# Kernel tuning notes

Hardware: AMD Instinct MI355X
Metric: run time of the kernel (lower is better)

## Reference

```python
import jax, jax.numpy as jnp
import numpy as np

BITS = 4
N_PACK = 32 // BITS  # int32 compression
GROUPSIZE = 128
MASK = (1 << BITS) - 1


def _unpack_int32(q, axis):
    """Unpack int32 tensor into N_PACK low-bit values along `axis`.
    Element j*N_PACK+e comes from bits [BITS*e, BITS*(e+1)) of packed word j."""
    parts = [ (q >> (BITS * e)) & MASK for e in range(N_PACK) ]
    u = jnp.stack(parts, axis=axis + 1)  # (..., P, N_PACK, ...)
    shape = list(q.shape)
    shape[axis] = shape[axis] * N_PACK
    return u.reshape(shape)


def setup_inputs() -> dict:
    key = jax.random.key(0)
    k1, k2, k3, k4, k5 = jax.random.split(key, 5)
    in_f, out_f = 4096, 12288
    tokens = 8192
    n_groups = in_f // GROUPSIZE  # 32
    x = jax.random.normal(k1, (tokens, in_f), dtype=jnp.float32)
    scales = jax.random.uniform(k2, (n_groups, out_f), dtype=jnp.float32) * 0.01 + 1e-3
    bias = jax.random.normal(k3, (out_f,), dtype=jnp.float32)
    qweight = jax.random.randint(k4, (in_f // N_PACK, out_f), jnp.iinfo(jnp.int32).min, jnp.iinfo(jnp.int32).max, dtype=jnp.int32)
    qzeros = jax.random.randint(k5, (n_groups, out_f // N_PACK), jnp.iinfo(jnp.int32).min, jnp.iinfo(jnp.int32).max, dtype=jnp.int32)
    return {"x": x, "scales": scales, "bias": bias, "qweight": qweight, "qzeros": qzeros}


def reference(x, scales, bias, qweight, qzeros):
    in_f = qweight.shape[0] * N_PACK
    out_f = qweight.shape[1]
    n_groups = scales.shape[0]
    # Unpack 4-bit weights along input-channel axis: (in_f, out_f), values 0..15
    w_int = _unpack_int32(qweight, axis=0).astype(scales.dtype)
    # Unpack zero points along output-channel axis; optimum format stores zp-1
    zp = (_unpack_int32(qzeros, axis=1) + 1).astype(scales.dtype)  # (n_groups, out_f)
    # Per-group dequant: group g covers input channels [g*GROUPSIZE, (g+1)*GROUPSIZE)
    w = (w_int.reshape(n_groups, GROUPSIZE, out_f) - zp[:, None, :]) * scales[:, None, :]
    w = w.reshape(in_f, out_f)
    # Linear: y = x @ W^T with W = w.T, i.e. x @ w
    return x @ w + bias
```

## Files before the change

kernel.cpp:

```cpp
#include <hip/hip_runtime.h>
#include <hip/hip_bf16.h>


typedef __attribute__((ext_vector_type(8))) short short8;
typedef __attribute__((ext_vector_type(4))) float f32x4;

__device__ __forceinline__ short f2bf(float f) {
  unsigned u = __float_as_uint(f);
  u += 0x7fffu + ((u >> 16) & 1u);
  return (short)(u >> 16);
}

__device__ __forceinline__ void gload_lds16(const void* g, void* l) {
  __builtin_amdgcn_global_load_lds(
      (const __attribute__((address_space(1))) void*)g,
      (__attribute__((address_space(3))) void*)l,
      16, 0, 0);
}

__device__ __forceinline__ void bar() {
  asm volatile("" ::: "memory");
  __builtin_amdgcn_s_barrier();
  asm volatile("" ::: "memory");
}

__global__ __launch_bounds__(256) void dequant_tile_kernel(
    const int* __restrict__ qweight, const int* __restrict__ qzeros,
    const float* __restrict__ scales, short* __restrict__ Bt,
    int N, int K) {
  const int ktn = K >> 5;
  const int bx = blockIdx.x;
  const int nb = bx / ktn, kt = bx - nb * ktn;
  const int t = threadIdx.x;
  const int g = kt >> 2;
  char* dst = (char*)Bt + (size_t)bx * 8192;
#pragma unroll
  for (int p = 0; p < 2; ++p) {
    const int c = p * 256 + t;
    const int l = c & 63;
    const int n = nb * 128 + (c >> 6) * 16 + (l & 15);
    const int kw = kt * 4 + (l >> 4);
    const float sc = scales[(size_t)g * N + n];
    const int zw = qzeros[(size_t)g * (N >> 3) + (n >> 3)];
    const float zs = -(float)(((zw >> ((n & 7) * 4)) & 15) + 1) * sc;
    const int w = qweight[(size_t)kw * N + n];
    short8 v;
#pragma unroll
    for (int e = 0; e < 8; ++e)
      v[e] = f2bf(fmaf((float)((w >> (4 * e)) & 15), sc, zs));
    *(short8*)(dst + c * 16) = v;
  }
}

__global__ __launch_bounds__(256) void cvt_tile_kernel(
    const float* __restrict__ x, short* __restrict__ xb, int K) {
  const int ktn = K >> 5;
  const int bx = blockIdx.x;
  const int mb = bx / ktn, kt = bx - mb * ktn;
  char* dst = (char*)xb + (size_t)bx * 16384;
#pragma unroll
  for (int p = 0; p < 4; ++p) {
    const int c = p * 256 + threadIdx.x;
    const int l = c & 63;
    const int row = mb * 256 + (c >> 6) * 16 + (l & 15);
    const int k = kt * 32 + (l >> 4) * 8;
    const float* s = x + (size_t)row * K + k;
    float4 f0 = *(const float4*)s;
    float4 f1 = *(const float4*)(s + 4);
    short8 v;
    v[0] = f2bf(f0.x); v[1] = f2bf(f0.y); v[2] = f2bf(f0.z); v[3] = f2bf(f0.w);
    v[4] = f2bf(f1.x); v[5] = f2bf(f1.y); v[6] = f2bf(f1.z); v[7] = f2bf(f1.w);
    *(short8*)(dst + c * 16) = v;
  }
}

#define GBM 256
#define GBN 128

__global__ __launch_bounds__(512, 4) void gemm256_kernel(
    const short* __restrict__ At, const short* __restrict__ Bt,
    const float* __restrict__ bias, float* __restrict__ C,
    int M, int N, int K) {
  __shared__ __align__(16) char lds[3 * 16384];
  const int tid = threadIdx.x;
  const int nbx = N / GBN;
  const int nwg = gridDim.x;
  int bid = blockIdx.x;
  if ((nwg & 7) == 0) bid = (bid & 7) * (nwg >> 3) + (bid >> 3);
  const int mb = bid / nbx;
  const int nb = bid % nbx;
  const int bm = mb * GBM, bn = nb * GBN;

  const int wid = tid >> 6, lane = tid & 63;
  const int wr = wid >> 1, wc = wid & 1;

  const int P = K >> 5;

  char* lb = &lds[0];

  const char* aBase = lb + wr * 4096 + lane * 16;

  const char* pA = (const char*)At + (size_t)mb * P * 16384 + (size_t)tid * 16;
  char* dA = lb + tid * 16;

  const char* pB = (const char*)Bt + (size_t)nb * P * 8192 + wc * 4096 +
                   (size_t)lane * 16;

  short8 bs[2][4];

#define STAGE(TSL, AOFF)                                 \
  do {                                                   \
    gload_lds16(pA + (AOFF), dA + (TSL)*16384);          \
    gload_lds16(pA + (AOFF) + 8192, dA + (TSL)*16384 + 8192); \
  } while (0)

#define LOADB(SET, BOFF)                                             \
  do {                                                               \
    asm volatile("global_load_dwordx4 %0, %1, off"                   \
                 : "=v"(bs[SET][0]) : "v"(pB + (BOFF)));             \
    asm volatile("global_load_dwordx4 %0, %1, off"                   \
                 : "=v"(bs[SET][1]) : "v"(pB + (BOFF) + 1024));      \
    asm volatile("global_load_dwordx4 %0, %1, off"                   \
                 : "=v"(bs[SET][2]) : "v"(pB + (BOFF) + 2048));      \
    asm volatile("global_load_dwordx4 %0, %1, off"                   \
                 : "=v"(bs[SET][3]) : "v"(pB + (BOFF) + 3072));      \
  } while (0)

#define WAITB(NSTR, SET)                                                   \
  asm volatile("s_waitcnt vmcnt(" NSTR ")"                                 \
               : "+v"(bs[SET][0]), "+v"(bs[SET][1]), "+v"(bs[SET][2]),     \
                 "+v"(bs[SET][3])::"memory")

  short8 aR[4];

#define RDA(SL)                                                   \
  do {                                                            \
    _Pragma("unroll") for (int i = 0; i < 4; ++i) aR[i] =         \
        *(const short8*)(aBase + (SL)*16384 + i * 1024);          \
  } while (0)

  f32x4 acc[4][4] = {};

#define MFMA16(SET)                                                      \
  do {                                                                   \
    __builtin_amdgcn_s_setprio(1);                                       \
    _Pragma("unroll") for (int i = 0; i < 4; ++i)                        \
        _Pragma("unroll") for (int j = 0; j < 4; ++j) acc[i][j] =        \
            __builtin_amdgcn_mfma_f32_16x16x32_bf16(aR[i], bs[SET][j],   \
                                                    acc[i][j], 0, 0, 0); \
    __builtin_amdgcn_s_setprio(0);                                       \
  } while (0)

#define PHASE(SL, SET, R)                                  \
  do {                                                     \
    WAITB("2", SET);                                       \
    bar();                                                 \
    RDA(SL);                                               \
    LOADB((SET) ^ 1, ((R) + 1) * 8192);                    \
    STAGE(((SL) + 2) % 3, ((R) + 2) * 16384);              \
    MFMA16(SET);                                           \
  } while (0)

  STAGE(0, 0);
  LOADB(0, 0);
  STAGE(1, 16384);

  const int nIt = (P - 2) / 6;
  for (int it = 0; it < nIt; ++it) {
    PHASE(0, 0, 0);
    PHASE(1, 1, 1);
    PHASE(2, 0, 2);
    PHASE(0, 1, 3);
    PHASE(1, 0, 4);
    PHASE(2, 1, 5);
    pA += 6 * 16384;
    pB += 6 * 8192;
  }
  WAITB("2", 0);
  bar();
  RDA(0);
  LOADB(1, 1 * 8192);
  MFMA16(0);
  WAITB("0", 1);
  bar();
  RDA(1);
  MFMA16(1);

#undef PHASE
#undef MFMA16
#undef RDA
#undef WAITB
#undef LOADB
#undef STAGE

  const int crow0 = bm + wr * 64 + (lane >> 4) * 4;
  const int ccol0 = bn + wc * 64 + (lane & 15);
#pragma unroll
  for (int fj = 0; fj < 4; ++fj) {
    const float bv = bias[ccol0 + fj * 16];
#pragma unroll
    for (int fi = 0; fi < 4; ++fi) {
#pragma unroll
      for (int r = 0; r < 4; ++r) {
        C[(size_t)(crow0 + fi * 16 + r) * N + ccol0 + fj * 16] =
            acc[fi][fj][r] + bv;
      }
    }
  }
}

__global__ __launch_bounds__(256) void dequant_kernel(
    const int* __restrict__ qweight, const int* __restrict__ qzeros,
    const float* __restrict__ scales, short* __restrict__ Wt,
    int in_f, int out_f) {
  __shared__ __align__(16) short T[64][72];
  const int n0 = blockIdx.x * 64;
  const int k0 = blockIdx.y * 64;
  const int t = threadIdx.x;
  const int nl = t & 63;
  const int kw = t >> 6;
  const int n = n0 + nl;
  const int g = k0 >> 7;
  const float sc = scales[(size_t)g * out_f + n];
  const int zpw = qzeros[(size_t)g * (out_f >> 3) + (n >> 3)];
  const float zp = (float)(((zpw >> ((n & 7) * 4)) & 15) + 1);
  const float zs = zp * sc;
#pragma unroll
  for (int rr = 0; rr < 2; ++rr) {
    const int kwi = kw + rr * 4;
    const int w = qweight[(size_t)((k0 >> 3) + kwi) * out_f + n];
    short8 v;
#pragma unroll
    for (int e = 0; e < 8; ++e) {
      float f = (float)((w >> (4 * e)) & 15) * sc - zs;
      v[e] = f2bf(f);
    }
    *(short8*)&T[nl][kwi * 8] = v;
  }
  __syncthreads();
#pragma unroll
  for (int rr = 0; rr < 2; ++rr) {
    const int c = rr * 256 + t;
    const int row = c >> 3, ch = c & 7;
    *(short8*)&Wt[(size_t)(n0 + row) * in_f + k0 + ch * 8] =
        *(const short8*)&T[row][ch * 8];
  }
}

__global__ __launch_bounds__(256) void cvt_kernel(
    const float* __restrict__ x, short* __restrict__ xb, long n8) {
  long i = (long)blockIdx.x * blockDim.x + threadIdx.x;
  if (i >= n8) return;
  const float* src = x + i * 8;
  float4 a = *(const float4*)src;
  float4 b = *(const float4*)(src + 4);
  short8 v;
  v[0] = f2bf(a.x); v[1] = f2bf(a.y); v[2] = f2bf(a.z); v[3] = f2bf(a.w);
  v[4] = f2bf(b.x); v[5] = f2bf(b.y); v[6] = f2bf(b.z); v[7] = f2bf(b.w);
  *(short8*)(xb + i * 8) = v;
}

#define BM 128
#define BN 128
#define BK 64

template <bool A_BF16>
__global__ __launch_bounds__(256) void gemm_bias_kernel(
    const void* __restrict__ Av, const short* __restrict__ Bt,
    const float* __restrict__ bias, float* __restrict__ C,
    int M, int N, int K) {
  __shared__ __align__(16) short As[BM * BK];
  __shared__ __align__(16) short Bs[BN * BK];
  const int tid = threadIdx.x;
  const int bm = blockIdx.y * BM;
  const int bn = blockIdx.x * BN;
  const int wid = tid >> 6, lane = tid & 63;
  const int wr = wid >> 1, wc = wid & 1;
  const int lrow = lane & 15;
  const int lk = (lane >> 4) * 8;

  f32x4 acc[4][4] = {};

  for (int kt = 0; kt < K; kt += BK) {
    if constexpr (A_BF16) {
      const short* A = (const short*)Av;
#pragma unroll
      for (int r = 0; r < 4; ++r) {
        const int c = r * 256 + tid;
        const int row = c >> 3, ch = c & 7;
        gload_lds16(A + (size_t)(bm + row) * K + kt + ch * 8,
                    (char*)As + c * 16);
      }
    } else {
      const float* A = (const float*)Av;
#pragma unroll
      for (int r = 0; r < 4; ++r) {
        const int c = r * 256 + tid;
        const int row = c >> 3, ch = c & 7;
        const float* src = A + (size_t)(bm + row) * K + kt + ch * 8;
        float4 f0 = *(const float4*)src;
        float4 f1 = *(const float4*)(src + 4);
        short8 v;
        v[0] = f2bf(f0.x); v[1] = f2bf(f0.y); v[2] = f2bf(f0.z); v[3] = f2bf(f0.w);
        v[4] = f2bf(f1.x); v[5] = f2bf(f1.y); v[6] = f2bf(f1.z); v[7] = f2bf(f1.w);
        *(short8*)((char*)As + c * 16) = v;
      }
    }
#pragma unroll
    for (int r = 0; r < 4; ++r) {
      const int c = r * 256 + tid;
      const int row = c >> 3, ch = c & 7;
      gload_lds16(Bt + (size_t)(bn + row) * K + kt + ch * 8,
                  (char*)Bs + c * 16);
    }
    __syncthreads();
#pragma unroll
    for (int kk = 0; kk < 2; ++kk) {
      short8 af[4], bf[4];
#pragma unroll
      for (int i = 0; i < 4; ++i)
        af[i] = *(const short8*)&As[(wr * 64 + i * 16 + lrow) * BK + kk * 32 + lk];
#pragma unroll
      for (int j = 0; j < 4; ++j)
        bf[j] = *(const short8*)&Bs[(wc * 64 + j * 16 + lrow) * BK + kk * 32 + lk];
#pragma unroll
      for (int i = 0; i < 4; ++i)
#pragma unroll
        for (int j = 0; j < 4; ++j)
          acc[i][j] = __builtin_amdgcn_mfma_f32_16x16x32_bf16(
              af[i], bf[j], acc[i][j], 0, 0, 0);
    }
    __syncthreads();
  }

  const int crow0 = bm + wr * 64 + (lane >> 4) * 4;
  const int ccol0 = bn + wc * 64 + (lane & 15);
#pragma unroll
  for (int j = 0; j < 4; ++j) {
    const float bv = bias[ccol0 + j * 16];
#pragma unroll
    for (int i = 0; i < 4; ++i) {
#pragma unroll
      for (int r = 0; r < 4; ++r) {
        C[(size_t)(crow0 + i * 16 + r) * N + ccol0 + j * 16] = acc[i][j][r] + bv;
      }
    }
  }
}

__global__ __launch_bounds__(256) void naive_kernel(
    const float* __restrict__ x, const float* __restrict__ scales,
    const float* __restrict__ bias, const int* __restrict__ qw,
    const int* __restrict__ qz, float* __restrict__ out,
    int M, int K, int N) {
  long idx = (long)blockIdx.x * blockDim.x + threadIdx.x;
  if (idx >= (long)M * N) return;
  const int n = (int)(idx % N);
  const int m = (int)(idx / N);
  float acc = 0.f;
  for (int g = 0; g < K / 128; ++g) {
    const float sc = scales[(size_t)g * N + n];
    const float zp =
        (float)(((qz[(size_t)g * (N >> 3) + (n >> 3)] >> ((n & 7) * 4)) & 15) + 1);
    const float zs = zp * sc;
    for (int kw = 0; kw < 16; ++kw) {
      const int w = qw[(size_t)(g * 16 + kw) * N + n];
      const float* xp = &x[(size_t)m * K + g * 128 + kw * 8];
#pragma unroll
      for (int e = 0; e < 8; ++e)
        acc += xp[e] * ((float)((w >> (4 * e)) & 15) * sc - zs);
    }
  }
  out[idx] = acc + bias[n];
}

extern "C" void kernel_launch(void* const* d_in, const int* in_sizes, int n_in,
                              void* d_out, int out_size, void* d_ws,
                              size_t ws_size, hipStream_t stream) {
  const float* x = (const float*)d_in[0];
  const float* scales = (const float*)d_in[1];
  const float* bias = (const float*)d_in[2];
  const int* qweight = (const int*)d_in[3];
  const int* qzeros = (const int*)d_in[4];
  float* out = (float*)d_out;

  const int out_f = in_sizes[2];
  const int kwords = in_sizes[3] / out_f;
  const int in_f = kwords * 8;
  const int tokens = in_sizes[0] / in_f;
  const int M = tokens, K = in_f, N = out_f;

  const size_t wt_bytes = (size_t)K * N * sizeof(short);
  const size_t xb_bytes = (size_t)M * K * sizeof(short);

  const bool div128 = (M % BM == 0) && (N % BN == 0) && (K % BK == 0) &&
                      (K % 128 == 0) && (N % 64 == 0);
  const bool divR19 = (M % GBM == 0) && (N % GBN == 0) && (K % 256 == 0) &&
                      (((K >> 5) - 2) % 6 == 0);

  if (divR19 && ws_size >= wt_bytes + xb_bytes) {
    short* Btile = (short*)d_ws;
    short* Atile = (short*)((char*)d_ws + wt_bytes);
    const int ktn = K >> 5;
    dequant_tile_kernel<<<(N / 128) * ktn, 256, 0, stream>>>(
        qweight, qzeros, scales, Btile, N, K);
    cvt_tile_kernel<<<(M / 256) * ktn, 256, 0, stream>>>(x, Atile, K);
    gemm256_kernel<<<(M / GBM) * (N / GBN), 512, 0, stream>>>(
        Atile, Btile, bias, out, M, N, K);
  } else if (div128 && ws_size >= wt_bytes + xb_bytes) {
    short* Wt = (short*)d_ws;
    short* xb = (short*)((char*)d_ws + wt_bytes);
    dequant_kernel<<<dim3(N / 64, K / 64), 256, 0, stream>>>(
        qweight, qzeros, scales, Wt, K, N);
    const long n8 = (long)M * K / 8;
    cvt_kernel<<<(int)((n8 + 255) / 256), 256, 0, stream>>>(x, xb, n8);
    gemm_bias_kernel<true><<<dim3(N / BN, M / BM), 256, 0, stream>>>(
        xb, Wt, bias, out, M, N, K);
  } else if (div128 && ws_size >= wt_bytes) {
    short* Wt = (short*)d_ws;
    dequant_kernel<<<dim3(N / 64, K / 64), 256, 0, stream>>>(
        qweight, qzeros, scales, Wt, K, N);
    gemm_bias_kernel<false><<<dim3(N / BN, M / BM), 256, 0, stream>>>(
        x, Wt, bias, out, M, N, K);
  } else {
    const long total = (long)M * N;
    naive_kernel<<<(int)((total + 255) / 256), 256, 0, stream>>>(
        x, scales, bias, qweight, qzeros, out, M, K, N);
  }
}
```

Baseline: 887.0 us.

## Swap operand paths: stream A via registers, stage B tiles through LDS

The GEMM previously staged the larger A tile (256 rows) through a triple-buffered LDS ring and loaded B fragments directly into registers. Now B (128 cols) goes through LDS with a smaller 24KB ring, and each wave loads its own A fragments straight from global memory into double-buffered registers. This cuts LDS footprint and LDS traffic per phase, which may allow higher occupancy. In exchange, A fragments are no longer shared through LDS, and the wait counts change to match one LDS load per phase.

```diff
diff --git a/kernel.cpp b/kernel.cpp
--- a/kernel.cpp
+++ b/kernel.cpp
@@ -81,7 +81,7 @@
     const short* __restrict__ At, const short* __restrict__ Bt,
     const float* __restrict__ bias, float* __restrict__ C,
     int M, int N, int K) {
-  __shared__ __align__(16) char lds[3 * 16384];
+  __shared__ __align__(16) char lds[3 * 8192];
   const int tid = threadIdx.x;
   const int nbx = N / GBN;
   const int nwg = gridDim.x;
@@ -98,45 +98,41 @@
 
   char* lb = &lds[0];
 
-  const char* aBase = lb + wr * 4096 + lane * 16;
-
-  const char* pA = (const char*)At + (size_t)mb * P * 16384 + (size_t)tid * 16;
-  char* dA = lb + tid * 16;
-
-  const char* pB = (const char*)Bt + (size_t)nb * P * 8192 + wc * 4096 +
+  const char* bBase = lb + wc * 4096 + lane * 16;
+
+  const char* pBs = (const char*)Bt + (size_t)nb * P * 8192 + (size_t)tid * 16;
+  char* dB = lb + tid * 16;
+
+  const char* pA = (const char*)At + (size_t)mb * P * 16384 + wr * 4096 +
                    (size_t)lane * 16;
 
-  short8 bs[2][4];
-
-#define STAGE(TSL, AOFF)                                 \
-  do {                                                   \
-    gload_lds16(pA + (AOFF), dA + (TSL)*16384);          \
-    gload_lds16(pA + (AOFF) + 8192, dA + (TSL)*16384 + 8192); \
-  } while (0)
-
-#define LOADB(SET, BOFF)                                             \
+  short8 aS[2][4];
+
+#define STAGEB(TSL, BOFF) gload_lds16(pBs + (BOFF), dB + (TSL)*8192)
+
+#define LOADA(SET, AOFF)                                             \
   do {                                                               \
     asm volatile("global_load_dwordx4 %0, %1, off"                   \
-                 : "=v"(bs[SET][0]) : "v"(pB + (BOFF)));             \
+                 : "=v"(aS[SET][0]) : "v"(pA + (AOFF)));             \
     asm volatile("global_load_dwordx4 %0, %1, off"                   \
-                 : "=v"(bs[SET][1]) : "v"(pB + (BOFF) + 1024));      \
+                 : "=v"(aS[SET][1]) : "v"(pA + (AOFF) + 1024));      \
     asm volatile("global_load_dwordx4 %0, %1, off"                   \
-                 : "=v"(bs[SET][2]) : "v"(pB + (BOFF) + 2048));      \
+                 : "=v"(aS[SET][2]) : "v"(pA + (AOFF) + 2048));      \
     asm volatile("global_load_dwordx4 %0, %1, off"                   \
-                 : "=v"(bs[SET][3]) : "v"(pB + (BOFF) + 3072));      \
+                 : "=v"(aS[SET][3]) : "v"(pA + (AOFF) + 3072));      \
   } while (0)
 
-#define WAITB(NSTR, SET)                                                   \
+#define WAITA(NSTR, SET)                                                   \
   asm volatile("s_waitcnt vmcnt(" NSTR ")"                                 \
-               : "+v"(bs[SET][0]), "+v"(bs[SET][1]), "+v"(bs[SET][2]),     \
-                 "+v"(bs[SET][3])::"memory")
-
-  short8 aR[4];
-
-#define RDA(SL)                                                   \
+               : "+v"(aS[SET][0]), "+v"(aS[SET][1]), "+v"(aS[SET][2]),     \
+                 "+v"(aS[SET][3])::"memory")
+
+  short8 bR[4];
+
+#define RDB(SL)                                                   \
   do {                                                            \
-    _Pragma("unroll") for (int i = 0; i < 4; ++i) aR[i] =         \
-        *(const short8*)(aBase + (SL)*16384 + i * 1024);          \
+    _Pragma("unroll") for (int j = 0; j < 4; ++j) bR[j] =         \
+        *(const short8*)(bBase + (SL)*8192 + j * 1024);           \
   } while (0)
 
   f32x4 acc[4][4] = {};
@@ -146,24 +142,24 @@
     __builtin_amdgcn_s_setprio(1);                                       \
     _Pragma("unroll") for (int i = 0; i < 4; ++i)                        \
         _Pragma("unroll") for (int j = 0; j < 4; ++j) acc[i][j] =        \
-            __builtin_amdgcn_mfma_f32_16x16x32_bf16(aR[i], bs[SET][j],   \
+            __builtin_amdgcn_mfma_f32_16x16x32_bf16(aS[SET][i], bR[j],   \
                                                     acc[i][j], 0, 0, 0); \
     __builtin_amdgcn_s_setprio(0);                                       \
   } while (0)
 
 #define PHASE(SL, SET, R)                                  \
   do {                                                     \
-    WAITB("2", SET);                                       \
+    WAITA("1", SET);                                       \
     bar();                                                 \
-    RDA(SL);                                               \
-    LOADB((SET) ^ 1, ((R) + 1) * 8192);                    \
-    STAGE(((SL) + 2) % 3, ((R) + 2) * 16384);              \
+    RDB(SL);                                               \
+    LOADA((SET) ^ 1, ((R) + 1) * 16384);                   \
+    STAGEB(((SL) + 2) % 3, ((R) + 2) * 8192);              \
     MFMA16(SET);                                           \
   } while (0)
 
-  STAGE(0, 0);
-  LOADB(0, 0);
-  STAGE(1, 16384);
+  LOADA(0, 0);
+  STAGEB(0, 0);
+  STAGEB(1, 8192);
 
   const int nIt = (P - 2) / 6;
   for (int it = 0; it < nIt; ++it) {
@@ -174,24 +170,24 @@
     PHASE(1, 0, 4);
     PHASE(2, 1, 5);
     pA += 6 * 16384;
-    pB += 6 * 8192;
-  }
-  WAITB("2", 0);
+    pBs += 6 * 8192;
+  }
+  WAITA("1", 0);
   bar();
-  RDA(0);
-  LOADB(1, 1 * 8192);
+  RDB(0);
+  LOADA(1, 1 * 16384);
   MFMA16(0);
-  WAITB("0", 1);
+  WAITA("0", 1);
   bar();
-  RDA(1);
+  RDB(1);
   MFMA16(1);
 
 #undef PHASE
 #undef MFMA16
-#undef RDA
-#undef WAITB
-#undef LOADB
-#undef STAGE
+#undef RDB
+#undef WAITA
+#undef LOADA
+#undef STAGEB
 
   const int crow0 = bm + wr * 64 + (lane >> 4) * 4;
   const int ccol0 = bn + wc * 64 + (lane & 15);
@@ -395,10 +391,10 @@
 
   const bool div128 = (M % BM == 0) && (N % BN == 0) && (K % BK == 0) &&
                       (K % 128 == 0) && (N % 64 == 0);
-  const bool divR19 = (M % GBM == 0) && (N % GBN == 0) && (K % 256 == 0) &&
+  const bool divR20 = (M % GBM == 0) && (N % GBN == 0) && (K % 256 == 0) &&
                       (((K >> 5) - 2) % 6 == 0);
 
-  if (divR19 && ws_size >= wt_bytes + xb_bytes) {
+  if (divR20 && ws_size >= wt_bytes + xb_bytes) {
     short* Btile = (short*)d_ws;
     short* Atile = (short*)((char*)d_ws + wt_bytes);
     const int ktn = K >> 5;
```

New measurement: 977.6 us. 10.2% more time.
